# Kernel tuning notes

Measured on AMD Instinct MI355X. Metric: run time of the kernel, lower is better.

Reference implementation:

```python
import jax, jax.numpy as jnp
import numpy as np

INPUT_DIM = 512
N_CLASSES = 100
N_SUBNETS = 20
HIDDEN = 32
WS1 = INPUT_DIM * HIDDEN   # 16384
BS1 = HIDDEN               # 32
WS2 = HIDDEN * N_CLASSES   # 3200
BS2 = N_CLASSES            # 100
TOTAL = WS1 + BS1 + WS2 + BS2  # 19716
LN_EPS = 1e-5


def _layernorm(v, g, b):
    mu = jnp.mean(v, axis=-1, keepdims=True)
    var = jnp.mean(jnp.square(v - mu), axis=-1, keepdims=True)
    return (v - mu) * jax.lax.rsqrt(var + LN_EPS) * g + b


def setup_inputs() -> dict:
    key = jax.random.key(0)
    ks = jax.random.split(key, 12)
    def lin(k, fan_in, shape):
        bound = 1.0 / np.sqrt(fan_in)
        return jax.random.uniform(k, shape, jnp.float32, -bound, bound)
    return {
        "x": jax.random.normal(ks[0], (32768, INPUT_DIM), jnp.float32),
        "W_h1": lin(ks[1], INPUT_DIM, (128, INPUT_DIM)),
        "b_h1": lin(ks[2], INPUT_DIM, (128,)),
        "g1": jnp.ones((128,), jnp.float32),
        "be1": jnp.zeros((128,), jnp.float32),
        "W_h2": lin(ks[3], 128, (256, 128)),
        "b_h2": lin(ks[4], 128, (256,)),
        "g2": jnp.ones((256,), jnp.float32),
        "be2": jnp.zeros((256,), jnp.float32),
        "W_h3": lin(ks[5], 256, (N_SUBNETS * TOTAL, 256)),
        "b_h3": lin(ks[6], 256, (N_SUBNETS * TOTAL,)),
        "ens_w": jnp.full((N_SUBNETS,), 1.0 / N_SUBNETS, jnp.float32),
    }


def reference(x, W_h1, b_h1, g1, be1, W_h2, b_h2, g2, be2, W_h3, b_h3, ens_w):
    # context from support set (= x itself): (1, input_dim)
    context = jnp.mean(x, axis=0, keepdims=True)
    # hypernet MLP (eval mode: dropout = identity)
    h = jax.nn.relu(_layernorm(context @ W_h1.T + b_h1, g1, be1))
    h = jax.nn.relu(_layernorm(h @ W_h2.T + b_h2, g2, be2))
    all_params = (h @ W_h3.T + b_h3).reshape(N_SUBNETS, TOTAL)
    # split generated params (same layout as torch .view)
    W1 = all_params[:, :WS1].reshape(N_SUBNETS, HIDDEN, INPUT_DIM)       # (S,H,I)
    b1 = all_params[:, WS1:WS1 + BS1]                                     # (S,H)
    W2 = all_params[:, WS1 + BS1:WS1 + BS1 + WS2].reshape(N_SUBNETS, N_CLASSES, HIDDEN)  # (S,C,H)
    b2 = all_params[:, WS1 + BS1 + WS2:]                                  # (S,C)
    # batched per-subnet 2-layer nets (dropout p=0.2 is identity in eval)
    hh = jax.nn.relu(jnp.einsum('bi,shi->sbh', x, W1) + b1[:, None, :])   # (S,B,H)
    logits = jnp.einsum('sbh,sch->sbc', hh, W2) + b2[:, None, :]          # (S,B,C)
    w = jax.nn.softmax(ens_w)                                             # (S,)
    return jnp.einsum('s,sbc->bc', w, logits)                             # (B,C)
```

## Files before the change

kernel.cpp:

```cpp
#include <hip/hip_runtime.h>
#include <hip/hip_bf16.h>

#define BATCH   32768
#define DIM     512
#define H1N     128
#define H2N     256
#define NSUB    20
#define HID     32
#define NCLS    100
#define NHID    640
#define TOTALP  19716
#define NPAR    394320
#define WS1P    16384
#define WS1B1   16416
#define WS2END  19616

#define OFF_PART 0
#define OFF_H    262144
#define OFF_W    262400
#define OFF_B1   262432
#define OFF_B2R  263072
#define OFF_W1B  265072
#define OFF_W2B  428912
#define OFF_PRED 470000

typedef __attribute__((ext_vector_type(8))) short short8;
typedef __attribute__((ext_vector_type(4))) float f32x4;

static __device__ inline unsigned short f2bf(float f) {
    __hip_bfloat16 h = __float2bfloat16(f);
    return *reinterpret_cast<unsigned short*>(&h);
}

static __device__ __forceinline__ void gload16(const void* g, void* l) {
    __builtin_amdgcn_global_load_lds(
        (const __attribute__((address_space(1))) void*)g,
        (__attribute__((address_space(3))) void*)l, 16, 0, 0);
}

__global__ __launch_bounds__(256) void k1_colsum(const float* __restrict__ x,
                                                 float* __restrict__ F) {
    __shared__ float sP[DIM];
    int t = threadIdx.x, bid = blockIdx.x;
    int par = t >> 7;
    int c4 = (t & 127) * 4;
    const float* xb = x + (size_t)bid * 64 * DIM;
    float4 acc = make_float4(0.f, 0.f, 0.f, 0.f);
    #pragma unroll 8
    for (int i = 0; i < 32; ++i) {
        int r = 2 * i + par;
        float4 v = *(const float4*)(xb + r * DIM + c4);
        acc.x += v.x; acc.y += v.y; acc.z += v.z; acc.w += v.w;
    }
    if (par == 0) *(float4*)(sP + c4) = acc;
    __syncthreads();
    if (par == 1) {
        float4 p = *(const float4*)(sP + c4);
        p.x += acc.x; p.y += acc.y; p.z += acc.z; p.w += acc.w;
        *(float4*)(F + OFF_PART + bid * DIM + c4) = p;
    }
}

__global__ __launch_bounds__(256) void k1b_red(float* __restrict__ F) {
    int bx = blockIdx.x;
    int orow = bx >> 1;
    int c = (bx & 1) * 256 + threadIdx.x;
    float s = 0.f;
    #pragma unroll 8
    for (int j = 0; j < 64; ++j)
        s += F[OFF_PART + (orow * 64 + j) * DIM + c];
    F[OFF_PRED + orow * DIM + c] = s;
}

__global__ __launch_bounds__(256) void k2_hyper(
    const float* __restrict__ Wh1, const float* __restrict__ bh1,
    const float* __restrict__ g1,  const float* __restrict__ be1,
    const float* __restrict__ Wh2, const float* __restrict__ bh2,
    const float* __restrict__ g2,  const float* __restrict__ be2,
    const float* __restrict__ ensw, float* __restrict__ F)
{
    __shared__ __align__(16) float sctx[DIM];
    __shared__ __align__(16) float sh1[H1N];
    __shared__ __align__(16) float sh2[H2N];
    int t = threadIdx.x;

    if (t < 128) {
        int c4 = t * 4;
        float4 a = make_float4(0.f, 0.f, 0.f, 0.f);
        #pragma unroll
        for (int b = 0; b < 8; ++b) {
            float4 v = *(const float4*)(F + OFF_PRED + b * DIM + c4);
            a.x += v.x; a.y += v.y; a.z += v.z; a.w += v.w;
        }
        a.x *= (1.0f / BATCH); a.y *= (1.0f / BATCH);
        a.z *= (1.0f / BATCH); a.w *= (1.0f / BATCH);
        *(float4*)(sctx + c4) = a;
    }
    __syncthreads();

    if (t < H1N) {
        float v = bh1[t];
        const float4* w = (const float4*)(Wh1 + t * DIM);
        for (int k = 0; k < DIM / 4; ++k) {
            float4 ww = w[k]; float4 c = *(const float4*)(sctx + k * 4);
            v += ww.x * c.x + ww.y * c.y + ww.z * c.z + ww.w * c.w;
        }
        sh1[t] = v;
    }
    __syncthreads();
    {
        float mu = 0.f;
        for (int k = 0; k < H1N; ++k) mu += sh1[k];
        mu *= (1.0f / H1N);
        float var = 0.f;
        for (int k = 0; k < H1N; ++k) { float d = sh1[k] - mu; var += d * d; }
        var *= (1.0f / H1N);
        float inv = rsqrtf(var + 1e-5f);
        __syncthreads();
        if (t < H1N) {
            float v = (sh1[t] - mu) * inv * g1[t] + be1[t];
            sh1[t] = fmaxf(v, 0.f);
        }
        __syncthreads();
    }

    {
        float v = bh2[t];
        const float4* w = (const float4*)(Wh2 + t * H1N);
        for (int k = 0; k < H1N / 4; ++k) {
            float4 ww = w[k]; float4 c = *(const float4*)(sh1 + k * 4);
            v += ww.x * c.x + ww.y * c.y + ww.z * c.z + ww.w * c.w;
        }
        sh2[t] = v;
    }
    __syncthreads();
    {
        float mu = 0.f;
        for (int k = 0; k < H2N; ++k) mu += sh2[k];
        mu *= (1.0f / H2N);
        float var = 0.f;
        for (int k = 0; k < H2N; ++k) { float d = sh2[k] - mu; var += d * d; }
        var *= (1.0f / H2N);
        float inv = rsqrtf(var + 1e-5f);
        float v = (sh2[t] - mu) * inv * g2[t] + be2[t];
        F[OFF_H + t] = fmaxf(v, 0.f);
    }

    if (t == 0) {
        float m = -1e30f;
        for (int s = 0; s < NSUB; ++s) m = fmaxf(m, ensw[s]);
        float sum = 0.f, e[NSUB];
        for (int s = 0; s < NSUB; ++s) { e[s] = __expf(ensw[s] - m); sum += e[s]; }
        for (int s = 0; s < NSUB; ++s) F[OFF_W + s] = e[s] / sum;
    }
}

static __device__ __forceinline__ void k3_pack(float* F, int row, float val) {
    __hip_bfloat16* W1B = (__hip_bfloat16*)(F + OFF_W1B);
    __hip_bfloat16* W2B = (__hip_bfloat16*)(F + OFF_W2B);
    int s = row / TOTALP;
    int r = row - s * TOTALP;
    if (r < WS1P) {
        int hh = r >> 9, k = r & 511;
        W1B[(s * HID + hh) * DIM + k] = __float2bfloat16(val);
    } else if (r < WS1B1) {
        F[OFF_B1 + s * HID + (r - WS1P)] = val;
    } else if (r < WS2END) {
        int q = r - WS1B1; int c = q >> 5, hh = q & 31;
        float ws = F[OFF_W + s];
        W2B[c * NHID + s * HID + hh] = __float2bfloat16(ws * val);
    } else {
        F[OFF_B2R + s * NCLS + (r - WS2END)] = val;
    }
}

#define K3_NWAVE 8192
#define K3_STRIDE (K3_NWAVE * 2)

__global__ __launch_bounds__(256) void k3_gemv(
    const float* __restrict__ Wh3, const float* __restrict__ bh3, float* __restrict__ F)
{
    int t = threadIdx.x;
    int wid = t >> 6, lane = t & 63;
    int gw = blockIdx.x * 4 + wid;
    const float4 h = *(const float4*)(F + OFF_H + lane * 4);

    int row = gw * 2;
    float4 w0, w1;
    if (row < NPAR) {
        w0 = *(const float4*)(Wh3 + (size_t)row * 256 + lane * 4);
        w1 = *(const float4*)(Wh3 + (size_t)(row + 1) * 256 + lane * 4);
    }
    while (row < NPAR) {
        int nrow = row + K3_STRIDE;
        float4 n0, n1;
        if (nrow < NPAR) {
            n0 = *(const float4*)(Wh3 + (size_t)nrow * 256 + lane * 4);
            n1 = *(const float4*)(Wh3 + (size_t)(nrow + 1) * 256 + lane * 4);
        }
        float d0 = w0.x * h.x + w0.y * h.y + w0.z * h.z + w0.w * h.w;
        float d1 = w1.x * h.x + w1.y * h.y + w1.z * h.z + w1.w * h.w;
        #pragma unroll
        for (int off = 32; off; off >>= 1) {
            d0 += __shfl_down(d0, off);
            d1 += __shfl_down(d1, off);
        }
        if (lane == 0) {
            k3_pack(F, row,     d0 + bh3[row]);
            k3_pack(F, row + 1, d1 + bh3[row + 1]);
        }
        w0 = n0; w1 = n1;
        row = nrow;
    }
}

__global__ __launch_bounds__(256) void gemm_fused(
    const float* __restrict__ x, const __hip_bfloat16* __restrict__ W1B,
    const __hip_bfloat16* __restrict__ W2B, const float* __restrict__ F,
    float* __restrict__ out)
{
    __shared__ __align__(16) unsigned char sB[2][128 * 128];
    __shared__ __align__(16) unsigned char sP[64 * 256];
    const int t = threadIdx.x;
    int bid = blockIdx.x;
    const int cpx = gridDim.x >> 3;
    bid = (bid & 7) * cpx + (bid >> 3);
    const int Row0 = bid * 64;
    const int wid = t >> 6, lane = t & 63;
    const int l16 = lane & 15, lq = lane >> 4;

    f32x4 acc1[8], acc2[8];
    #pragma unroll
    for (int fn = 0; fn < 8; ++fn) acc2[fn] = (f32x4){0.f, 0.f, 0.f, 0.f};

    auto stageW1 = [&](int n1, int kc, int b) {
        #pragma unroll
        for (int i = 0; i < 4; ++i) {
            int cidx = wid * 4 + i;
            int ul = cidx * 64 + lane;
            int row = ul >> 3, u = ul & 7;
            gload16(W1B + (size_t)(n1 * 128 + row) * 512 + kc + ((u ^ (row & 7)) << 3),
                    &sB[b][cidx * 1024]);
        }
    };
    auto stageW2 = [&](int n1, int h, int b) {
        #pragma unroll
        for (int i = 0; i < 4; ++i) {
            int cidx = wid * 4 + i;
            int ul = cidx * 64 + lane;
            int row = ul >> 3, u = ul & 7;
            gload16(W2B + (size_t)row * NHID + n1 * 128 + h * 64 + ((u ^ (row & 7)) << 3),
                    &sB[b][cidx * 1024]);
        }
    };

    stageW1(0, 0, 0);

    short8 afr[16];
    {
        const float* xrow = x + (size_t)(Row0 + wid * 16 + l16) * 512;
        #pragma unroll
        for (int i = 0; i < 16; ++i) {
            int k0 = (i >> 1) * 64 + (i & 1) * 32 + lq * 8;
            float4 a = *(const float4*)(xrow + k0);
            float4 b = *(const float4*)(xrow + k0 + 4);
            unsigned int p[4];
            p[0] = (unsigned)f2bf(a.x) | ((unsigned)f2bf(a.y) << 16);
            p[1] = (unsigned)f2bf(a.z) | ((unsigned)f2bf(a.w) << 16);
            p[2] = (unsigned)f2bf(b.x) | ((unsigned)f2bf(b.y) << 16);
            p[3] = (unsigned)f2bf(b.z) | ((unsigned)f2bf(b.w) << 16);
            afr[i] = *(short8*)p;
        }
    }
    asm volatile("s_waitcnt vmcnt(0)" ::: "memory");
    __builtin_amdgcn_s_barrier();

    auto comp1 = [&](int st, int b) {
        #pragma unroll
        for (int kk = 0; kk < 2; ++kk) {
            int u = kk * 4 + lq;
            short8 af = afr[st * 2 + kk];
            short8 bfv[8];
            #pragma unroll
            for (int fn = 0; fn < 8; ++fn) {
                int rw = fn * 16 + l16;
                bfv[fn] = *(const short8*)(&sB[b][rw * 128 + ((u ^ (rw & 7)) << 4)]);
            }
            #pragma unroll
            for (int fn = 0; fn < 8; ++fn)
                acc1[fn] = __builtin_amdgcn_mfma_f32_16x16x32_bf16(
                    af, bfv[fn], acc1[fn], 0, 0, 0);
        }
    };
    auto comp2 = [&](int h, int b) {
        #pragma unroll
        for (int kk = 0; kk < 2; ++kk) {
            int u = kk * 4 + lq;
            int punit = (h * 2 + kk) * 4 + lq;
            int arow = wid * 16 + l16;
            short8 af = *(const short8*)(&sP[arow * 256 + ((punit ^ (arow & 7)) << 4)]);
            short8 bfv[8];
            #pragma unroll
            for (int fn = 0; fn < 8; ++fn) {
                int rw = fn * 16 + l16;
                bfv[fn] = *(const short8*)(&sB[b][rw * 128 + ((u ^ (rw & 7)) << 4)]);
            }
            #pragma unroll
            for (int fn = 0; fn < 8; ++fn)
                acc2[fn] = __builtin_amdgcn_mfma_f32_16x16x32_bf16(
                    af, bfv[fn], acc2[fn], 0, 0, 0);
        }
    };

    int buf = 0;
    float b1r[8];
    for (int n1 = 0; n1 < 5; ++n1) {
        #pragma unroll
        for (int st = 0; st < 10; ++st) {
            if (st < 9) {
                if (st + 1 < 8) stageW1(n1, (st + 1) * 64, buf ^ 1);
                else stageW2(n1, st + 1 - 8, buf ^ 1);
            } else if (n1 < 4) {
                stageW1(n1 + 1, 0, buf ^ 1);
            }
            if (st == 9 && n1 == 4)
                asm volatile("s_waitcnt vmcnt(0)" ::: "memory");
            else
                asm volatile("s_waitcnt vmcnt(4)" ::: "memory");
            __builtin_amdgcn_s_barrier();
            __builtin_amdgcn_sched_barrier(0);

            if (st == 0) {
                #pragma unroll
                for (int fn = 0; fn < 8; ++fn) {
                    acc1[fn] = (f32x4){0.f, 0.f, 0.f, 0.f};
                    b1r[fn] = F[OFF_B1 + n1 * 128 + fn * 16 + l16];
                }
            }
            if (st < 8) comp1(st, buf);
            else comp2(st - 8, buf);
            if (st == 7) {
                #pragma unroll
                for (int fn = 0; fn < 8; ++fn) {
                    int col = fn * 16 + l16;
                    int unit = col >> 3;
                    #pragma unroll
                    for (int r = 0; r < 4; ++r) {
                        int row = wid * 16 + lq * 4 + r;
                        float v = fmaxf(acc1[fn][r] + b1r[fn], 0.f);
                        *(unsigned short*)(&sP[row * 256 + ((unit ^ (row & 7)) << 4)
                                           + (col & 7) * 2]) = f2bf(v);
                    }
                }
            }
            __builtin_amdgcn_sched_barrier(0);
            __builtin_amdgcn_s_barrier();
            buf ^= 1;
        }
    }

    float* sBe = (float*)sP;
    if (t < 128) {
        float b = 0.f;
        if (t < NCLS) {
            #pragma unroll
            for (int s = 0; s < NSUB; ++s)
                b += F[OFF_W + s] * F[OFF_B2R + s * NCLS + t];
        }
        sBe[t] = b;
    }
    __syncthreads();

    #pragma unroll
    for (int fn = 0; fn < 8; ++fn) {
        int gcol = fn * 16 + l16;
        if (gcol < NCLS) {
            float be = sBe[gcol];
            #pragma unroll
            for (int r = 0; r < 4; ++r) {
                int grow = Row0 + wid * 16 + lq * 4 + r;
                out[(size_t)grow * NCLS + gcol] = acc2[fn][r] + be;
            }
        }
    }
}

extern "C" void kernel_launch(void* const* d_in, const int* in_sizes, int n_in,
                              void* d_out, int out_size, void* d_ws, size_t ws_size,
                              hipStream_t stream)
{
    const float* x    = (const float*)d_in[0];
    const float* Wh1  = (const float*)d_in[1];
    const float* bh1  = (const float*)d_in[2];
    const float* g1   = (const float*)d_in[3];
    const float* be1  = (const float*)d_in[4];
    const float* Wh2  = (const float*)d_in[5];
    const float* bh2  = (const float*)d_in[6];
    const float* g2   = (const float*)d_in[7];
    const float* be2  = (const float*)d_in[8];
    const float* Wh3  = (const float*)d_in[9];
    const float* bh3  = (const float*)d_in[10];
    const float* ensw = (const float*)d_in[11];
    float* F = (float*)d_ws;
    float* out = (float*)d_out;

    const __hip_bfloat16* W1B = (const __hip_bfloat16*)(F + OFF_W1B);
    const __hip_bfloat16* W2B = (const __hip_bfloat16*)(F + OFF_W2B);

    k1_colsum<<<512, 256, 0, stream>>>(x, F);
    k1b_red<<<16, 256, 0, stream>>>(F);
    k2_hyper<<<1, 256, 0, stream>>>(Wh1, bh1, g1, be1, Wh2, bh2, g2, be2, ensw, F);
    k3_gemv<<<2048, 256, 0, stream>>>(Wh3, bh3, F);
    gemm_fused<<<BATCH / 64, 256, 0, stream>>>(x, W1B, W2B, F, out);
}
```

Before: 177.6 us.

## Double K-chunk size in fused GEMM pipeline to halve barrier stages

Widens each staged weight chunk from 64 to 128 K-elements, doubling the LDS buffers to 64KB and restructuring the 50-step pipeline into 25 steps. Each step issues 8 async loads and 4 MFMA k-substeps, aiming to halve the barrier and waitcnt overhead per tile. The cost is more LDS per block, which may reduce occupancy, and a deeper wait queue. The x fragment indexing is adjusted so the K ordering matches.

Result: slower. 200.1 us (+12.6%).

```diff
diff --git a/kernel.cpp b/kernel.cpp
--- a/kernel.cpp
+++ b/kernel.cpp
@@ -219,7 +219,7 @@
     const __hip_bfloat16* __restrict__ W2B, const float* __restrict__ F,
     float* __restrict__ out)
 {
-    __shared__ __align__(16) unsigned char sB[2][128 * 128];
+    __shared__ __align__(16) unsigned char sB[2][128 * 256];
     __shared__ __align__(16) unsigned char sP[64 * 256];
     const int t = threadIdx.x;
     int bid = blockIdx.x;
@@ -235,22 +235,20 @@
 
     auto stageW1 = [&](int n1, int kc, int b) {
         #pragma unroll
-        for (int i = 0; i < 4; ++i) {
-            int cidx = wid * 4 + i;
-            int ul = cidx * 64 + lane;
-            int row = ul >> 3, u = ul & 7;
+        for (int i = 0; i < 8; ++i) {
+            int ul = (wid * 8 + i) * 64 + lane;
+            int row = ul >> 4, u = ul & 15;
             gload16(W1B + (size_t)(n1 * 128 + row) * 512 + kc + ((u ^ (row & 7)) << 3),
-                    &sB[b][cidx * 1024]);
+                    &sB[b][(wid * 8 + i) * 1024]);
         }
     };
-    auto stageW2 = [&](int n1, int h, int b) {
-        #pragma unroll
-        for (int i = 0; i < 4; ++i) {
-            int cidx = wid * 4 + i;
-            int ul = cidx * 64 + lane;
-            int row = ul >> 3, u = ul & 7;
-            gload16(W2B + (size_t)row * NHID + n1 * 128 + h * 64 + ((u ^ (row & 7)) << 3),
-                    &sB[b][cidx * 1024]);
+    auto stageW2 = [&](int n1, int b) {
+        #pragma unroll
+        for (int i = 0; i < 8; ++i) {
+            int ul = (wid * 8 + i) * 64 + lane;
+            int row = ul >> 4, u = ul & 15;
+            gload16(W2B + (size_t)row * NHID + n1 * 128 + ((u ^ (row & 7)) << 3),
+                    &sB[b][(wid * 8 + i) * 1024]);
         }
     };
 
@@ -261,7 +259,7 @@
         const float* xrow = x + (size_t)(Row0 + wid * 16 + l16) * 512;
         #pragma unroll
         for (int i = 0; i < 16; ++i) {
-            int k0 = (i >> 1) * 64 + (i & 1) * 32 + lq * 8;
+            int k0 = i * 32 + lq * 8;
             float4 a = *(const float4*)(xrow + k0);
             float4 b = *(const float4*)(xrow + k0 + 4);
             unsigned int p[4];
@@ -277,14 +275,14 @@
 
     auto comp1 = [&](int st, int b) {
         #pragma unroll
-        for (int kk = 0; kk < 2; ++kk) {
+        for (int kk = 0; kk < 4; ++kk) {
             int u = kk * 4 + lq;
-            short8 af = afr[st * 2 + kk];
+            short8 af = afr[st * 4 + kk];
             short8 bfv[8];
             #pragma unroll
             for (int fn = 0; fn < 8; ++fn) {
                 int rw = fn * 16 + l16;
-                bfv[fn] = *(const short8*)(&sB[b][rw * 128 + ((u ^ (rw & 7)) << 4)]);
+                bfv[fn] = *(const short8*)(&sB[b][rw * 256 + ((u ^ (rw & 7)) << 4)]);
             }
             #pragma unroll
             for (int fn = 0; fn < 8; ++fn)
@@ -292,18 +290,17 @@
                     af, bfv[fn], acc1[fn], 0, 0, 0);
         }
     };
-    auto comp2 = [&](int h, int b) {
-        #pragma unroll
-        for (int kk = 0; kk < 2; ++kk) {
+    auto comp2 = [&](int b) {
+        #pragma unroll
+        for (int kk = 0; kk < 4; ++kk) {
             int u = kk * 4 + lq;
-            int punit = (h * 2 + kk) * 4 + lq;
             int arow = wid * 16 + l16;
-            short8 af = *(const short8*)(&sP[arow * 256 + ((punit ^ (arow & 7)) << 4)]);
+            short8 af = *(const short8*)(&sP[arow * 256 + ((u ^ (arow & 7)) << 4)]);
             short8 bfv[8];
             #pragma unroll
             for (int fn = 0; fn < 8; ++fn) {
                 int rw = fn * 16 + l16;
-                bfv[fn] = *(const short8*)(&sB[b][rw * 128 + ((u ^ (rw & 7)) << 4)]);
+                bfv[fn] = *(const short8*)(&sB[b][rw * 256 + ((u ^ (rw & 7)) << 4)]);
             }
             #pragma unroll
             for (int fn = 0; fn < 8; ++fn)
@@ -314,49 +311,44 @@
 
     int buf = 0;
     float b1r[8];
-    for (int n1 = 0; n1 < 5; ++n1) {
-        #pragma unroll
-        for (int st = 0; st < 10; ++st) {
-            if (st < 9) {
-                if (st + 1 < 8) stageW1(n1, (st + 1) * 64, buf ^ 1);
-                else stageW2(n1, st + 1 - 8, buf ^ 1);
-            } else if (n1 < 4) {
-                stageW1(n1 + 1, 0, buf ^ 1);
+    for (int p = 0; p < 25; ++p) {
+        int n1 = p / 5, st = p % 5;
+        if (p < 24) {
+            int np = p + 1, nn1 = np / 5, nst = np % 5;
+            if (nst < 4) stageW1(nn1, nst * 128, buf ^ 1);
+            else stageW2(nn1, buf ^ 1);
+        }
+        if (p < 24) asm volatile("s_waitcnt vmcnt(8)" ::: "memory");
+        else        asm volatile("s_waitcnt vmcnt(0)" ::: "memory");
+        __builtin_amdgcn_s_barrier();
+        __builtin_amdgcn_sched_barrier(0);
+
+        if (st == 0) {
+            #pragma unroll
+            for (int fn = 0; fn < 8; ++fn) {
+                acc1[fn] = (f32x4){0.f, 0.f, 0.f, 0.f};
+                b1r[fn] = F[OFF_B1 + n1 * 128 + fn * 16 + l16];
             }
-            if (st == 9 && n1 == 4)
-                asm volatile("s_waitcnt vmcnt(0)" ::: "memory");
-            else
-                asm volatile("s_waitcnt vmcnt(4)" ::: "memory");
-            __builtin_amdgcn_s_barrier();
-            __builtin_amdgcn_sched_barrier(0);
-
-            if (st == 0) {
+        }
+        if (st < 4) comp1(st, buf);
+        else comp2(buf);
+        if (st == 3) {
+            #pragma unroll
+            for (int fn = 0; fn < 8; ++fn) {
+                int col = fn * 16 + l16;
+                int unit = col >> 3;
                 #pragma unroll
-                for (int fn = 0; fn < 8; ++fn) {
-                    acc1[fn] = (f32x4){0.f, 0.f, 0.f, 0.f};
-                    b1r[fn] = F[OFF_B1 + n1 * 128 + fn * 16 + l16];
+                for (int r = 0; r < 4; ++r) {
+                    int row = wid * 16 + lq * 4 + r;
+                    float v = fmaxf(acc1[fn][r] + b1r[fn], 0.f);
+                    *(unsigned short*)(&sP[row * 256 + ((unit ^ (row & 7)) << 4)
+                                       + (col & 7) * 2]) = f2bf(v);
                 }
             }
-            if (st < 8) comp1(st, buf);
-            else comp2(st - 8, buf);
-            if (st == 7) {
-                #pragma unroll
-                for (int fn = 0; fn < 8; ++fn) {
-                    int col = fn * 16 + l16;
-                    int unit = col >> 3;
-                    #pragma unroll
-                    for (int r = 0; r < 4; ++r) {
-                        int row = wid * 16 + lq * 4 + r;
-                        float v = fmaxf(acc1[fn][r] + b1r[fn], 0.f);
-                        *(unsigned short*)(&sP[row * 256 + ((unit ^ (row & 7)) << 4)
-                                           + (col & 7) * 2]) = f2bf(v);
-                    }
-                }
-            }
-            __builtin_amdgcn_sched_barrier(0);
-            __builtin_amdgcn_s_barrier();
-            buf ^= 1;
-        }
+        }
+        __builtin_amdgcn_sched_barrier(0);
+        __builtin_amdgcn_s_barrier();
+        buf ^= 1;
     }
 
     float* sBe = (float*)sP;
```
